# Kernel optimization log

Hardware: AMD Instinct MI355X
Metric: run time of the kernel (lower is better)

## Reference

```python
import jax, jax.numpy as jnp
import numpy as np

E, D_IN, D_HID, D_OUT, N = 8, 1024, 2048, 1024, 8192


def setup_inputs() -> dict:
    key = jax.random.key(0)
    ks = jax.random.split(key, 9)
    s_in = 1.0 / np.sqrt(D_IN)
    s_hid = 1.0 / np.sqrt(D_HID)
    return {
        "x": jax.random.normal(ks[0], (N, D_IN), dtype=jnp.float32),
        "gW": jax.random.normal(ks[1], (D_IN, E), dtype=jnp.float32) * s_in,
        "gb": jnp.zeros((E,), dtype=jnp.float32),
        "W0": jax.random.normal(ks[2], (E, D_IN, D_HID), dtype=jnp.float32) * s_in,
        "b0": jax.random.normal(ks[3], (E, D_HID), dtype=jnp.float32) * 0.01,
        "W1": jax.random.normal(ks[4], (E, D_HID, D_HID), dtype=jnp.float32) * s_hid,
        "b1": jax.random.normal(ks[5], (E, D_HID), dtype=jnp.float32) * 0.01,
        "Wf": jax.random.normal(ks[6], (E, D_HID, D_OUT), dtype=jnp.float32) * s_hid,
        "bf": jax.random.normal(ks[7], (E, D_OUT), dtype=jnp.float32) * 0.01,
    }


def reference(x, gW, gb, W0, b0, W1, b1, Wf, bf):
    # gate: softmax over experts  [N, E]
    gate = jax.nn.softmax(x @ gW + gb, axis=-1)
    # all experts densely, batched over expert axis E
    h = jax.nn.relu(jnp.einsum("nd,edh->enh", x, W0) + b0[:, None, :])   # [E,N,H]
    h = jax.nn.relu(jnp.einsum("enh,ehk->enk", h, W1) + b1[:, None, :])  # [E,N,H]
    o = jnp.einsum("enh,eho->eno", h, Wf) + bf[:, None, :]               # [E,N,O]
    # gate-weighted sum over experts -> [N, O]
    return jnp.einsum("ne,eno->no", gate, o)
```

## Files before the change

### kernel.cpp

```cpp
#include <hip/hip_runtime.h>
#include <hip/hip_bf16.h>


typedef short s16x8 __attribute__((ext_vector_type(8)));
typedef float f32x4 __attribute__((ext_vector_type(4)));

#define E_ 8
#define DIN_ 1024
#define DH_ 2048
#define DOUT_ 1024
#define NTOK_ 8192

__device__ __forceinline__ unsigned short f2bf(float x) {
    union { float f; unsigned u; } c; c.f = x;
    unsigned r = c.u + 0x7fffu + ((c.u >> 16) & 1u);
    return (unsigned short)(r >> 16);
}
__device__ __forceinline__ float bf2f(unsigned short s) {
    union { unsigned u; float f; } c; c.u = ((unsigned)s) << 16;
    return c.f;
}
__device__ __forceinline__ void gload_lds16(const void* g, void* l) {
    __builtin_amdgcn_global_load_lds((const __attribute__((address_space(1))) void*)g,
                                     (__attribute__((address_space(3))) void*)l, 16, 0, 0);
}

__global__ __launch_bounds__(256) void cvt_f32_bf16(const float* __restrict__ in,
                                                    unsigned short* __restrict__ out,
                                                    long n8) {
    long i = (long)blockIdx.x * 256 + threadIdx.x;
    if (i >= n8) return;
    const float4* p = (const float4*)(in + i * 8);
    float4 a = p[0], b = p[1];
    s16x8 v;
    v[0] = (short)f2bf(a.x); v[1] = (short)f2bf(a.y);
    v[2] = (short)f2bf(a.z); v[3] = (short)f2bf(a.w);
    v[4] = (short)f2bf(b.x); v[5] = (short)f2bf(b.y);
    v[6] = (short)f2bf(b.z); v[7] = (short)f2bf(b.w);
    *(s16x8*)(out + i * 8) = v;
}

__global__ __launch_bounds__(256) void tcvt_kernel(const float* __restrict__ in,
                                                   unsigned short* __restrict__ out,
                                                   int K, int Nn) {
    __shared__ unsigned short t[64][72];
    const int e = blockIdx.z;
    const float* ie = in + (long)e * K * Nn;
    unsigned short* oe = out + (long)e * K * Nn;
    const int k0 = blockIdx.y * 64, n0 = blockIdx.x * 64;
    const int tid = threadIdx.x;
    const int c4 = (tid & 15) * 4;
#pragma unroll
    for (int i = 0; i < 4; ++i) {
        const int k = (tid >> 4) + 16 * i;
        float4 v = *(const float4*)(ie + (long)(k0 + k) * Nn + n0 + c4);
        t[c4 + 0][k] = f2bf(v.x);
        t[c4 + 1][k] = f2bf(v.y);
        t[c4 + 2][k] = f2bf(v.z);
        t[c4 + 3][k] = f2bf(v.w);
    }
    __syncthreads();
#pragma unroll
    for (int i = 0; i < 2; ++i) {
        const int idx = tid + 256 * i;
        const int rn = idx >> 3, ck = idx & 7;
        s16x8 v = *(const s16x8*)&t[rn][ck * 8];
        *(s16x8*)(oe + (long)(n0 + rn) * K + k0 + ck * 8) = v;
    }
}

__global__ __launch_bounds__(256) void gate_kernel(const float* __restrict__ x,
                                                   const float* __restrict__ gW,
                                                   const float* __restrict__ gb,
                                                   float* __restrict__ gate) {
    __shared__ float gws[8 * 1024];
    const int tid = threadIdx.x;
    for (int idx = tid; idx < 8 * 1024; idx += 256)
        gws[(idx & 7) * 1024 + (idx >> 3)] = gW[idx];
    __syncthreads();
    const int w = tid >> 6, l = tid & 63;
    const int n = blockIdx.x * 4 + w;
    const float* xr = x + (long)n * 1024;
    float acc[8] = {};
    for (int k = l; k < 1024; k += 64) {
        const float xv = xr[k];
#pragma unroll
        for (int e = 0; e < 8; ++e) acc[e] += xv * gws[e * 1024 + k];
    }
#pragma unroll
    for (int e = 0; e < 8; ++e)
        for (int off = 32; off > 0; off >>= 1) acc[e] += __shfl_xor(acc[e], off);
    if (l == 0) {
        float m = -1e30f;
#pragma unroll
        for (int e = 0; e < 8; ++e) { acc[e] += gb[e]; m = fmaxf(m, acc[e]); }
        float s = 0.f;
#pragma unroll
        for (int e = 0; e < 8; ++e) { acc[e] = __expf(acc[e] - m); s += acc[e]; }
        const float inv = 1.0f / s;
#pragma unroll
        for (int e = 0; e < 8; ++e) gate[n * 8 + e] = acc[e] * inv;
    }
}


#define BARR() asm volatile("s_barrier" ::: "memory")
#define LGKM0() do { asm volatile("s_waitcnt lgkmcnt(0)" ::: "memory"); \
                     __builtin_amdgcn_sched_barrier(0); } while (0)
#define VMW(n) do { asm volatile("s_waitcnt vmcnt(" #n ")" ::: "memory"); \
                    __builtin_amdgcn_sched_barrier(0); } while (0)

__global__ __launch_bounds__(512, 2) void moe_gemm256(const unsigned short* __restrict__ A,
                                                      const unsigned short* __restrict__ Bt,
                                                      const float* __restrict__ bias,
                                                      unsigned short* __restrict__ out,
                                                      int M, int Nn, int K,
                                                      long sAe, long sBe, long sOe, int relu) {
    extern __shared__ char smem[];
    const int tid = threadIdx.x;
    const int l = tid & 63, wid = tid >> 6;
    const int wr = wid >> 2, wc = wid & 3;
    const int e = blockIdx.z;
    const int gx = gridDim.x;
    int lin = blockIdx.x + gx * blockIdx.y;
    {
        const int nwg = gx * gridDim.y;
        const int q = nwg >> 3, r = nwg & 7;
        const int xcd = lin & 7, idx = lin >> 3;
        lin = (xcd < r ? xcd * (q + 1) : r * (q + 1) + (xcd - r) * q) + idx;
    }
    const int n0 = (lin % gx) * 256;
    const int m0 = (lin / gx) * 256;

    const unsigned short* Ae = A + (long)e * sAe;
    const unsigned short* Be = Bt + (long)e * sBe;

    const int srow = wid * 8 + (l >> 3);
    const int sc8 = ((l & 7) ^ (l >> 3)) * 8;
    const unsigned short* pA = Ae + (long)(m0 + srow) * K + sc8;
    const unsigned short* pB = Be + (long)(n0 + srow) * K + sc8;
    const long kst64 = 64L * K;
    char* ldsW = smem + wid * 1024;

#define STAGE_A(buf, half, kt) do { \
        const unsigned short* s_ = pA + (long)(half) * 128 * K + (long)(kt) * 64; \
        char* d_ = ldsW + (buf) * 65536 + (half) * 16384; \
        gload_lds16(s_, d_); gload_lds16(s_ + kst64, d_ + 8192); } while (0)
#define STAGE_B(buf, half, kt) do { \
        const unsigned short* s_ = pB + (long)(half) * 128 * K + (long)(kt) * 64; \
        char* d_ = ldsW + (buf) * 65536 + 32768 + (half) * 16384; \
        gload_lds16(s_, d_); gload_lds16(s_ + kst64, d_ + 8192); } while (0)

    const int arow = l & 15;
    const int aswz = ((l >> 4) ^ (l & 7)) << 4;
    const int aoffb = wr * 16384 + arow * 128;
    const int boffb = 32768 + wc * 8192 + arow * 128;

    f32x4 acc[8][4] = {};
    s16x8 af[4][2], bf0[2][2], bf1[2][2];

#define LDA(buf, mhalf) do { \
        const char* p_ = smem + (buf) * 65536 + aoffb + (mhalf) * 8192; \
        _Pragma("unroll") for (int mi_ = 0; mi_ < 4; ++mi_) \
        _Pragma("unroll") for (int kk_ = 0; kk_ < 2; ++kk_) \
            af[mi_][kk_] = *(const s16x8*)(p_ + mi_ * 2048 + (aswz ^ (kk_ << 6))); } while (0)
#define LDB(buf, nhalf, dst) do { \
        const char* p_ = smem + (buf) * 65536 + boffb + (nhalf) * 4096; \
        _Pragma("unroll") for (int ni_ = 0; ni_ < 2; ++ni_) \
        _Pragma("unroll") for (int kk_ = 0; kk_ < 2; ++kk_) \
            dst[ni_][kk_] = *(const s16x8*)(p_ + ni_ * 2048 + (aswz ^ (kk_ << 6))); } while (0)
#define MFMA8(mb, nb, bfr) do { __builtin_amdgcn_s_setprio(1); \
        _Pragma("unroll") for (int mi_ = 0; mi_ < 4; ++mi_) \
        _Pragma("unroll") for (int ni_ = 0; ni_ < 2; ++ni_) \
        _Pragma("unroll") for (int kk_ = 0; kk_ < 2; ++kk_) \
            acc[(mb) + mi_][(nb) + ni_] = __builtin_amdgcn_mfma_f32_16x16x32_bf16( \
                af[mi_][kk_], bfr[ni_][kk_], acc[(mb) + mi_][(nb) + ni_], 0, 0, 0); \
        __builtin_amdgcn_s_setprio(0); __builtin_amdgcn_sched_barrier(0); } while (0)

    const int nit = K >> 7;

    STAGE_A(0, 0, 0); STAGE_A(0, 1, 0); STAGE_B(0, 0, 0); STAGE_B(0, 1, 0);
    STAGE_B(1, 0, 1); STAGE_A(1, 0, 1);
    VMW(4);
    BARR();
    LDA(0, 0); LDB(0, 0, bf0);

    for (int it = 0; it < nit; ++it) {
        const int ktY = 2 * it + 1;
        const int ktX2 = (it + 1 < nit) ? 2 * it + 2 : 0;
        const int ktY2 = (it + 1 < nit) ? 2 * it + 3 : 1;
        LGKM0(); MFMA8(0, 0, bf0);
        STAGE_A(1, 1, ktY);
        LDB(0, 1, bf1);
        BARR(); LGKM0(); MFMA8(0, 2, bf1);
        STAGE_B(1, 1, ktY);
        LDA(0, 1);
        BARR(); LGKM0(); MFMA8(4, 2, bf1);
        STAGE_B(0, 0, ktX2);
        BARR(); MFMA8(4, 0, bf0);
        STAGE_B(0, 1, ktX2);
        VMW(4);
        BARR();
        LDA(1, 0); LDB(1, 0, bf0);
        LGKM0(); MFMA8(0, 0, bf0);
        STAGE_A(0, 0, ktX2);
        LDB(1, 1, bf1);
        BARR(); LGKM0(); MFMA8(0, 2, bf1);
        STAGE_A(0, 1, ktX2);
        LDA(1, 1);
        BARR(); LGKM0(); MFMA8(4, 2, bf1);
        STAGE_B(1, 0, ktY2);
        BARR(); MFMA8(4, 0, bf0);
        STAGE_A(1, 0, ktY2);
        VMW(4);
        BARR();
        LDA(0, 0); LDB(0, 0, bf0);
    }
    LGKM0();
    VMW(0);
    BARR();

    unsigned short* oe = out + (long)e * sOe;
    const float* be = bias + (long)e * Nn;
    float bv[4];
#pragma unroll
    for (int ni = 0; ni < 4; ++ni) bv[ni] = be[n0 + 64 * wc + 16 * ni + arow];
    unsigned short (*h)[272] = (unsigned short (*)[272])smem;
#pragma unroll
    for (int p = 0; p < 2; ++p) {
        if (p) BARR();
        if (wr == p) {
#pragma unroll
            for (int mi = 0; mi < 8; ++mi)
#pragma unroll
                for (int ni = 0; ni < 4; ++ni) {
                    const int col = 64 * wc + 16 * ni + arow;
                    const int rl = 16 * mi + (l >> 4) * 4;
#pragma unroll
                    for (int j = 0; j < 4; ++j) {
                        float xv = acc[mi][ni][j] + bv[ni];
                        if (relu) xv = fmaxf(xv, 0.0f);
                        h[rl + j][col] = f2bf(xv);
                    }
                }
        }
        BARR();
#pragma unroll
        for (int i = 0; i < 8; ++i) {
            const int lin2 = i * 512 + tid;
            const int row = lin2 >> 5, ch = (lin2 & 31) * 8;
            s16x8 v = *(const s16x8*)&h[row][ch];
            *(s16x8*)(oe + (long)(m0 + 128 * p + row) * Nn + n0 + ch) = v;
        }
    }
#undef STAGE_A
#undef STAGE_B
#undef LDA
#undef LDB
#undef MFMA8
}

template <int FUSE>
__global__ __launch_bounds__(256) void moe_gemm(const unsigned short* __restrict__ A,
                                                const unsigned short* __restrict__ Bt,
                                                const float* __restrict__ bias,
                                                void* __restrict__ outp,
                                                const float* __restrict__ gate8,
                                                int M, int Nn, int K,
                                                long strideAe, long strideBe, long strideOe,
                                                int relu, int first) {
    __shared__ __align__(16) char smem[34816];
    const int tid = threadIdx.x;
    const int w = tid >> 6, l = tid & 63;
    const int e = blockIdx.z;
    const int m0 = blockIdx.y * 128;
    const int n0 = blockIdx.x * 128;

    const unsigned short* Ae = A + (long)e * strideAe;
    const unsigned short* Be = Bt + (long)e * strideBe;

    const int srow = tid >> 2;
    const int scol = (tid & 3) * 8;
    const unsigned short* gA = Ae + (long)(m0 + srow) * K + scol;
    const unsigned short* gB = Be + (long)(n0 + srow) * K + scol;
    const long rstep = (long)64 * K;

    char* ldsAw = smem + w * 1024;
    char* ldsBw = smem + 8192 + w * 1024;

    const int wr = w >> 1, wc = w & 1;
    const int lr = l & 15;
    const int aoff = (64 * wr + lr) * 64 + (l >> 4) * 16;
    const int boff = 8192 + (64 * wc + lr) * 64 + (l >> 4) * 16;

    f32x4 acc[4][4] = {};
    const int nt = K >> 5;

    gload_lds16(gA, ldsAw);
    gload_lds16(gA + rstep, ldsAw + 4096);
    gload_lds16(gB, ldsBw);
    gload_lds16(gB + rstep, ldsBw + 4096);
    __syncthreads();

    int cur = 0;
    for (int t = 0; t < nt; ++t) {
        if (t + 1 < nt) {
            const int nb = (cur ^ 1) * 16384;
            const unsigned short* a = gA + (t + 1) * 32;
            const unsigned short* b = gB + (t + 1) * 32;
            gload_lds16(a, ldsAw + nb);
            gload_lds16(a + rstep, ldsAw + nb + 4096);
            gload_lds16(b, ldsBw + nb);
            gload_lds16(b + rstep, ldsBw + nb + 4096);
        }
        const char* buf = smem + cur * 16384;
        s16x8 af[4], bfr[4];
#pragma unroll
        for (int m = 0; m < 4; ++m) af[m] = *(const s16x8*)(buf + aoff + m * 1024);
#pragma unroll
        for (int n = 0; n < 4; ++n) bfr[n] = *(const s16x8*)(buf + boff + n * 1024);
#pragma unroll
        for (int m = 0; m < 4; ++m)
#pragma unroll
            for (int n = 0; n < 4; ++n)
                acc[m][n] = __builtin_amdgcn_mfma_f32_16x16x32_bf16(af[m], bfr[n], acc[m][n], 0, 0, 0);
        __syncthreads();
        cur ^= 1;
    }

    const float* be = bias + (long)e * Nn;

    if constexpr (!FUSE) {
        unsigned short (*h)[136] = (unsigned short (*)[136])smem;
#pragma unroll
        for (int n = 0; n < 4; ++n) {
            const int lc = 64 * wc + 16 * n + lr;
            const float bb = be[n0 + lc];
#pragma unroll
            for (int m = 0; m < 4; ++m) {
                const int rbase = 64 * wr + 16 * m + (l >> 4) * 4;
                f32x4 v = acc[m][n];
#pragma unroll
                for (int j = 0; j < 4; ++j) {
                    float xv = v[j] + bb;
                    if (relu) xv = fmaxf(xv, 0.0f);
                    h[rbase + j][lc] = f2bf(xv);
                }
            }
        }
        __syncthreads();
        unsigned short* oe = (unsigned short*)outp + (long)e * strideOe;
#pragma unroll
        for (int it = 0; it < 8; ++it) {
            const int row = (tid >> 4) + 16 * it;
            const int ch = tid & 15;
            s16x8 v = *(const s16x8*)&h[row][ch * 8];
            *(s16x8*)(oe + (long)(m0 + row) * Nn + n0 + ch * 8) = v;
        }
    } else {
        float* outf = (float*)outp;
        float (*h2)[132] = (float (*)[132])smem;
#pragma unroll
        for (int p2 = 0; p2 < 2; ++p2) {
            if (p2) __syncthreads();
            if (wr == p2) {
#pragma unroll
                for (int n = 0; n < 4; ++n) {
                    const int lc = 64 * wc + 16 * n + lr;
                    const float bb = be[n0 + lc];
#pragma unroll
                    for (int m = 0; m < 4; ++m) {
                        const int rloc = 16 * m + (l >> 4) * 4;
                        f32x4 v = acc[m][n];
#pragma unroll
                        for (int j = 0; j < 4; ++j) h2[rloc + j][lc] = v[j] + bb;
                    }
                }
            }
            __syncthreads();
#pragma unroll
            for (int it = 0; it < 8; ++it) {
                const int lin = it * 256 + tid;
                const int row = lin >> 5;
                const int c4 = (lin & 31) * 4;
                const long grow = (long)m0 + p2 * 64 + row;
                const float g = gate8[grow * 8];
                float* op = outf + grow * Nn + n0 + c4;
                float4 hv = *(const float4*)&h2[row][c4];
                float4 r;
                if (first) {
                    r = make_float4(g * hv.x, g * hv.y, g * hv.z, g * hv.w);
                } else {
                    float4 o0 = *(const float4*)op;
                    r = make_float4(o0.x + g * hv.x, o0.y + g * hv.y,
                                    o0.z + g * hv.z, o0.w + g * hv.w);
                }
                *(float4*)op = r;
            }
        }
    }
}

__global__ __launch_bounds__(256) void combine_kernel(const unsigned short* __restrict__ o,
                                                      const float* __restrict__ gate,
                                                      float* __restrict__ out, int Nc) {
    const long t = (long)blockIdx.x * 256 + threadIdx.x;
    const int n = (int)(t >> 7);
    const int ch = (int)(t & 127) * 8;
    float g[8];
#pragma unroll
    for (int e = 0; e < 8; ++e) g[e] = gate[n * 8 + e];
    float a[8] = {};
#pragma unroll
    for (int e = 0; e < 8; ++e) {
        s16x8 v = *(const s16x8*)(o + (long)e * Nc * DOUT_ + (long)n * DOUT_ + ch);
        const float ge = g[e];
#pragma unroll
        for (int j = 0; j < 8; ++j) a[j] = fmaf(ge, bf2f((unsigned short)v[j]), a[j]);
    }
    float* op = out + (long)n * DOUT_ + ch;
    *(float4*)(op) = make_float4(a[0], a[1], a[2], a[3]);
    *(float4*)(op + 4) = make_float4(a[4], a[5], a[6], a[7]);
}

extern "C" void kernel_launch(void* const* d_in, const int* in_sizes, int n_in,
                              void* d_out, int out_size, void* d_ws, size_t ws_size,
                              hipStream_t stream) {
    const float* x   = (const float*)d_in[0];
    const float* gW  = (const float*)d_in[1];
    const float* gb  = (const float*)d_in[2];
    const float* W0  = (const float*)d_in[3];
    const float* b0  = (const float*)d_in[4];
    const float* W1  = (const float*)d_in[5];
    const float* b1  = (const float*)d_in[6];
    const float* Wf  = (const float*)d_in[7];
    const float* bfb = (const float*)d_in[8];
    float* out = (float*)d_out;
    char* ws = (char*)d_ws;

    unsigned short* xb = (unsigned short*)ws;
    float* gate = (float*)(ws + (size_t)NTOK_ * DIN_ * 2);
    const size_t base = (size_t)NTOK_ * DIN_ * 2 + (size_t)NTOK_ * E_ * 4;

    const size_t wfull = (size_t)E_ * 2 * ((size_t)DIN_ * DH_ + (size_t)DH_ * DH_ + (size_t)DH_ * DOUT_);
    const size_t wexp = wfull / E_;

    int Nc = 0, batched = 0;
    if (ws_size > base + wfull) {
        const size_t rem = ws_size - base - wfull;
        for (int nc = 8192; nc >= 256; nc >>= 1)
            if ((size_t)nc * 65536 <= rem) { Nc = nc; batched = 1; break; }
    }
    if (!batched) {
        const size_t rem = (ws_size > base + wexp) ? ws_size - base - wexp : 0;
        for (int nc = 8192; nc >= 128; nc >>= 1)
            if ((size_t)nc * 8192 <= rem) { Nc = nc; break; }
        if (!Nc) Nc = 128;
    }
    const int nch = NTOK_ / Nc;

    cvt_f32_bf16<<<NTOK_ * DIN_ / 8 / 256, 256, 0, stream>>>(x, xb, (long)NTOK_ * DIN_ / 8);
    gate_kernel<<<NTOK_ / 4, 256, 0, stream>>>(x, gW, gb, gate);

    if (batched) {
        hipFuncSetAttribute(reinterpret_cast<const void*>(&moe_gemm256),
                            hipFuncAttributeMaxDynamicSharedMemorySize, 131072);
        unsigned short* W0b = (unsigned short*)(ws + base);
        unsigned short* W1b = W0b + (size_t)E_ * DIN_ * DH_;
        unsigned short* Wfb = W1b + (size_t)E_ * DH_ * DH_;
        unsigned short* h0  = Wfb + (size_t)E_ * DH_ * DOUT_;
        unsigned short* h1  = h0 + (size_t)E_ * Nc * DH_;
        tcvt_kernel<<<dim3(DH_ / 64, DIN_ / 64, E_), 256, 0, stream>>>(W0, W0b, DIN_, DH_);
        tcvt_kernel<<<dim3(DH_ / 64, DH_ / 64, E_), 256, 0, stream>>>(W1, W1b, DH_, DH_);
        tcvt_kernel<<<dim3(DOUT_ / 64, DH_ / 64, E_), 256, 0, stream>>>(Wf, Wfb, DH_, DOUT_);
        for (int c = 0; c < nch; ++c) {
            const long r0 = (long)c * Nc;
            moe_gemm256<<<dim3(DH_ / 256, Nc / 256, E_), 512, 131072, stream>>>(
                xb + r0 * DIN_, W0b, b0, h0, Nc, DH_, DIN_,
                0L, (long)DIN_ * DH_, (long)Nc * DH_, 1);
            moe_gemm256<<<dim3(DH_ / 256, Nc / 256, E_), 512, 131072, stream>>>(
                h0, W1b, b1, h1, Nc, DH_, DH_,
                (long)Nc * DH_, (long)DH_ * DH_, (long)Nc * DH_, 1);
            unsigned short* o = h0;
            moe_gemm256<<<dim3(DOUT_ / 256, Nc / 256, E_), 512, 131072, stream>>>(
                h1, Wfb, bfb, o, Nc, DOUT_, DH_,
                (long)Nc * DH_, (long)DH_ * DOUT_, (long)Nc * DOUT_, 0);
            combine_kernel<<<Nc / 2, 256, 0, stream>>>(o, gate + r0 * E_, out + r0 * DOUT_, Nc);
        }
    } else {
        unsigned short* W0s = (unsigned short*)(ws + base);
        unsigned short* W1s = W0s + (size_t)DIN_ * DH_;
        unsigned short* Wfs = W1s + (size_t)DH_ * DH_;
        unsigned short* h0s = Wfs + (size_t)DH_ * DOUT_;
        unsigned short* h1s = h0s + (size_t)Nc * DH_;
        for (int e = 0; e < E_; ++e) {
            tcvt_kernel<<<dim3(DH_ / 64, DIN_ / 64, 1), 256, 0, stream>>>(
                W0 + (size_t)e * DIN_ * DH_, W0s, DIN_, DH_);
            tcvt_kernel<<<dim3(DH_ / 64, DH_ / 64, 1), 256, 0, stream>>>(
                W1 + (size_t)e * DH_ * DH_, W1s, DH_, DH_);
            tcvt_kernel<<<dim3(DOUT_ / 64, DH_ / 64, 1), 256, 0, stream>>>(
                Wf + (size_t)e * DH_ * DOUT_, Wfs, DH_, DOUT_);
            for (int c = 0; c < nch; ++c) {
                const long r0 = (long)c * Nc;
                moe_gemm<0><<<dim3(DH_ / 128, Nc / 128, 1), 256, 0, stream>>>(
                    xb + r0 * DIN_, W0s, b0 + e * DH_, h0s, nullptr, Nc, DH_, DIN_,
                    0L, 0L, 0L, 1, 0);
                moe_gemm<0><<<dim3(DH_ / 128, Nc / 128, 1), 256, 0, stream>>>(
                    h0s, W1s, b1 + e * DH_, h1s, nullptr, Nc, DH_, DH_,
                    0L, 0L, 0L, 1, 0);
                moe_gemm<1><<<dim3(DOUT_ / 128, Nc / 128, 1), 256, 0, stream>>>(
                    h1s, Wfs, bfb + e * DOUT_, out + r0 * DOUT_, gate + r0 * E_ + e,
                    Nc, DOUT_, DH_, 0L, 0L, 0L, 0, (e == 0) ? 1 : 0);
            }
        }
    }
}
```

Baseline: 1.126 ms.

## Merge MFMA phases into two per half-tile with fewer barriers

Restructures the GEMM main loop so each half K-tile runs two larger MFMA clusters (32 MFMAs each) instead of four 16-MFMA clusters. Both B fragments are loaded up front, and the global-to-LDS staging is regrouped, with one A stage moved earlier and the vmcnt waits adjusted to match. This halves the barriers and priority toggles per iteration, cutting sync overhead. The trade-offs are higher register pressure and coarser overlap between memory staging and compute.

New measurement: 1.168 ms. +3.7%, slower.

```diff
diff --git a/kernel.cpp b/kernel.cpp
--- a/kernel.cpp
+++ b/kernel.cpp
@@ -169,52 +169,44 @@
         _Pragma("unroll") for (int ni_ = 0; ni_ < 2; ++ni_) \
         _Pragma("unroll") for (int kk_ = 0; kk_ < 2; ++kk_) \
             dst[ni_][kk_] = *(const s16x8*)(p_ + ni_ * 2048 + (aswz ^ (kk_ << 6))); } while (0)
-#define MFMA8(mb, nb, bfr) do { __builtin_amdgcn_s_setprio(1); \
+#define MFMA8(mb, nb, bfr) do { \
         _Pragma("unroll") for (int mi_ = 0; mi_ < 4; ++mi_) \
         _Pragma("unroll") for (int ni_ = 0; ni_ < 2; ++ni_) \
         _Pragma("unroll") for (int kk_ = 0; kk_ < 2; ++kk_) \
             acc[(mb) + mi_][(nb) + ni_] = __builtin_amdgcn_mfma_f32_16x16x32_bf16( \
-                af[mi_][kk_], bfr[ni_][kk_], acc[(mb) + mi_][(nb) + ni_], 0, 0, 0); \
-        __builtin_amdgcn_s_setprio(0); __builtin_amdgcn_sched_barrier(0); } while (0)
+                af[mi_][kk_], bfr[ni_][kk_], acc[(mb) + mi_][(nb) + ni_], 0, 0, 0); } while (0)
+#define PRIO1() __builtin_amdgcn_s_setprio(1)
+#define PRIO0() do { __builtin_amdgcn_s_setprio(0); \
+                     __builtin_amdgcn_sched_barrier(0); } while (0)
 
     const int nit = K >> 7;
 
     STAGE_A(0, 0, 0); STAGE_A(0, 1, 0); STAGE_B(0, 0, 0); STAGE_B(0, 1, 0);
-    STAGE_B(1, 0, 1); STAGE_A(1, 0, 1);
-    VMW(4);
+    STAGE_B(1, 0, 1);
+    VMW(2);
     BARR();
-    LDA(0, 0); LDB(0, 0, bf0);
+    LDA(0, 0); LDB(0, 0, bf0); LDB(0, 1, bf1);
 
     for (int it = 0; it < nit; ++it) {
         const int ktY = 2 * it + 1;
         const int ktX2 = (it + 1 < nit) ? 2 * it + 2 : 0;
         const int ktY2 = (it + 1 < nit) ? 2 * it + 3 : 1;
-        LGKM0(); MFMA8(0, 0, bf0);
-        STAGE_A(1, 1, ktY);
-        LDB(0, 1, bf1);
-        BARR(); LGKM0(); MFMA8(0, 2, bf1);
-        STAGE_B(1, 1, ktY);
+        LGKM0(); PRIO1(); MFMA8(0, 0, bf0); MFMA8(0, 2, bf1); PRIO0();
+        STAGE_A(1, 1, ktY); STAGE_B(1, 1, ktY); STAGE_A(1, 0, ktY);
         LDA(0, 1);
-        BARR(); LGKM0(); MFMA8(4, 2, bf1);
-        STAGE_B(0, 0, ktX2);
-        BARR(); MFMA8(4, 0, bf0);
-        STAGE_B(0, 1, ktX2);
+        BARR(); LGKM0(); PRIO1(); MFMA8(4, 2, bf1); MFMA8(4, 0, bf0); PRIO0();
+        STAGE_B(0, 0, ktX2); STAGE_B(0, 1, ktX2);
         VMW(4);
         BARR();
-        LDA(1, 0); LDB(1, 0, bf0);
-        LGKM0(); MFMA8(0, 0, bf0);
-        STAGE_A(0, 0, ktX2);
-        LDB(1, 1, bf1);
-        BARR(); LGKM0(); MFMA8(0, 2, bf1);
-        STAGE_A(0, 1, ktX2);
+        LDA(1, 0); LDB(1, 0, bf0); LDB(1, 1, bf1);
+        LGKM0(); PRIO1(); MFMA8(0, 0, bf0); MFMA8(0, 2, bf1); PRIO0();
+        STAGE_A(0, 0, ktX2); STAGE_A(0, 1, ktX2);
         LDA(1, 1);
-        BARR(); LGKM0(); MFMA8(4, 2, bf1);
+        BARR(); LGKM0(); PRIO1(); MFMA8(4, 2, bf1); MFMA8(4, 0, bf0); PRIO0();
         STAGE_B(1, 0, ktY2);
-        BARR(); MFMA8(4, 0, bf0);
-        STAGE_A(1, 0, ktY2);
-        VMW(4);
+        VMW(2);
         BARR();
-        LDA(0, 0); LDB(0, 0, bf0);
+        LDA(0, 0); LDB(0, 0, bf0); LDB(0, 1, bf1);
     }
     LGKM0();
     VMW(0);
```
